# Kernel optimization log

Hardware: AMD Instinct MI355X
Metric: run time of the kernel (lower is better)

## Reference

```python
import jax, jax.numpy as jnp
import numpy as np

R_MAX = 5.0
P_CUT = 5
NAVG = 16.0
L_OF_LM = np.array([0, 1, 1, 1, 2, 2, 2, 2, 2, 3, 3, 3, 3, 3, 3, 3])


def _sph(v):
    # real spherical harmonics up to l=3 on normalized vectors, [E,16]
    n = jnp.sqrt(jnp.sum(v * v, -1, keepdims=True) + 1e-12)
    u = v / n
    x, y, z = u[..., 0], u[..., 1], u[..., 2]
    s3, s15, s5 = np.sqrt(3.0), np.sqrt(15.0), np.sqrt(5.0)
    s70, s105, s42, s7 = np.sqrt(70.0), np.sqrt(105.0), np.sqrt(42.0), np.sqrt(7.0)
    Y = [jnp.ones_like(x),
         s3 * x, s3 * y, s3 * z,
         s15 * x * y, s15 * y * z, 0.5 * s5 * (3 * z * z - 1.0), s15 * x * z, 0.5 * s15 * (x * x - y * y),
         0.25 * s70 * y * (3 * x * x - y * y), s105 * x * y * z, 0.25 * s42 * y * (5 * z * z - 1.0),
         0.5 * s7 * z * (5 * z * z - 3.0), 0.25 * s42 * x * (5 * z * z - 1.0),
         0.5 * s105 * z * (x * x - y * y), 0.25 * s70 * x * (3 * x * x - y * y)]
    return jnp.stack(Y, -1)


def _radial(r):
    # Bessel basis * smooth polynomial cutoff, r: [E] -> [E, 8]
    n = jnp.arange(1, 9, dtype=r.dtype)
    bess = np.sqrt(2.0 / R_MAX) * jnp.sin(n * np.pi * r[:, None] / R_MAX) / (r[:, None] + 1e-9)
    u = r / R_MAX
    p = float(P_CUT)
    f = 1.0 - 0.5 * (p + 1) * (p + 2) * u ** P_CUT + p * (p + 2) * u ** (P_CUT + 1) - 0.5 * p * (p + 1) * u ** (P_CUT + 2)
    f = jnp.where(u < 1.0, f, 0.0)
    return bess * f[:, None]


def _energy(node_attrs, positions, shifts, atomic_energies, W_embed, W_up, W_r1, W_r2, W_r3,
            W_lin, W_skip, U1, U2, U3, Wc1, Wc2, Wc3, W_prod, W_readout,
            edge_index, batch, num_graphs):
    send, recv = edge_index[0], edge_index[1]
    vec = positions[recv] - positions[send] + shifts
    r = jnp.sqrt(jnp.sum(vec * vec, -1) + 1e-12)
    Y = _sph(vec)                       # [E,16]
    edge_feats = _radial(r)             # [E,8]
    h = node_attrs @ W_embed            # [N,K] scalar node features
    lidx = jnp.asarray(L_OF_LM)
    N = h.shape[0]
    for i in range(2):
        h_up = h @ W_up[i]
        w = jax.nn.silu(edge_feats @ W_r1[i])
        w = jax.nn.silu(w @ W_r2[i])
        w = (w @ W_r3[i]).reshape(edge_feats.shape[0], -1, 4)   # [E,K,4] per-l radial tp weights
        w_lm = w[:, :, lidx]                                    # [E,K,16]
        m = w_lm * h_up[send][:, :, None] * Y[:, None, :]       # scalar x SH tensor product messages
        agg = jax.ops.segment_sum(m, recv, num_segments=N) / NAVG
        Wm = W_lin[i][lidx]                                     # [16,K,K] per-l linear
        mixed = jnp.einsum('nkm,mkh->nhm', agg, Wm)
        sc = jnp.einsum('nk,ne,ekh->nh', h, node_attrs, W_skip[i])  # element-wise skip tp -> scalars
        A = mixed.at[:, :, 0].add(sc)                           # [N,K,16] A-basis
        # ACE symmetric product basis (invariant outputs), element-dependent weights
        w1 = jnp.einsum('ne,epk->npk', node_attrs, Wc1[i])
        b1 = jnp.einsum('nkp,npk->nk', jnp.einsum('nka,ap->nkp', A, U1), w1)
        AA = jnp.einsum('nka,nkb->nkab', A, A)                  # [N,K,16,16]
        w2 = jnp.einsum('ne,epk->npk', node_attrs, Wc2[i])
        b2 = jnp.einsum('nkp,npk->nk', jnp.einsum('nkab,abp->nkp', AA, U2), w2)
        T3 = jnp.einsum('nkab,abcp->nkcp', AA, U3)              # [N,K,16,8]
        w3 = jnp.einsum('ne,epk->npk', node_attrs, Wc3[i])
        b3 = jnp.einsum('nkp,npk->nk', jnp.einsum('nkcp,nkc->nkp', T3, A), w3)
        h = (b1 + b2 + b3) @ W_prod[i]
    node_es = h @ W_readout                                     # [N]
    node_e0 = node_attrs @ atomic_energies
    e0 = jax.ops.segment_sum(node_e0, batch, num_segments=num_graphs)
    inter = jax.ops.segment_sum(node_es, batch, num_segments=num_graphs)
    return e0 + inter


def setup_inputs():
    key = jax.random.key(0)
    ks = jax.random.split(key, 24)
    N, E, K, NE, G, NB = 2048, 32768, 128, 10, 16, 8
    P1, P2, P3, L = 2, 4, 8, 16

    def rn(k, shape, fan):
        return jax.random.normal(k, shape, jnp.float32) / np.sqrt(fan)

    elem = jax.random.randint(ks[0], (N,), 0, NE)
    return {
        'node_attrs': jax.nn.one_hot(elem, NE, dtype=jnp.float32),
        'positions': jax.random.uniform(ks[1], (N, 3), jnp.float32) * 6.0,
        'shifts': jnp.zeros((E, 3), jnp.float32),
        'atomic_energies': jax.random.normal(ks[2], (NE,), jnp.float32),
        'W_embed': rn(ks[3], (NE, K), NE),
        'W_up': rn(ks[4], (2, K, K), K),
        'W_r1': rn(ks[5], (2, NB, 64), NB),
        'W_r2': rn(ks[6], (2, 64, 64), 64),
        'W_r3': rn(ks[7], (2, 64, K * 4), 64),
        'W_lin': rn(ks[8], (2, 4, K, K), K),
        'W_skip': rn(ks[9], (2, NE, K, K), K),
        'U1': rn(ks[10], (L, P1), L),
        'U2': rn(ks[11], (L, L, P2), L * L),
        'U3': rn(ks[12], (L, L, L, P3), L * L * L),
        'Wc1': rn(ks[13], (2, NE, P1, K), P1),
        'Wc2': rn(ks[14], (2, NE, P2, K), P2),
        'Wc3': rn(ks[15], (2, NE, P3, K), P3),
        'W_prod': rn(ks[16], (2, K, K), K),
        'W_readout': rn(ks[17], (K,), K),
        'edge_index': jax.random.randint(ks[18], (2, E), 0, N).astype(jnp.int32),
        'batch': jnp.sort(jax.random.randint(ks[19], (N,), 0, G)).astype(jnp.int32),
        'num_graphs': 16,
    }


def reference(node_attrs, positions, shifts, atomic_energies, W_embed, W_up, W_r1, W_r2, W_r3,
              W_lin, W_skip, U1, U2, U3, Wc1, Wc2, Wc3, W_prod, W_readout,
              edge_index, batch, num_graphs):
    e_fn = lambda pos: _energy(node_attrs, pos, shifts, atomic_energies, W_embed, W_up, W_r1, W_r2,
                               W_r3, W_lin, W_skip, U1, U2, U3, Wc1, Wc2, Wc3, W_prod, W_readout,
                               edge_index, batch, num_graphs)
    energy = e_fn(positions)
    forces = -jax.grad(lambda p: e_fn(p).sum())(positions)
    return energy, forces
```

## Files before the change

kernel.cpp:

```cpp
#include <hip/hip_runtime.h>
#include <math.h>

#define KCH 128
#define NELEM 10

__device__ __forceinline__ int lidxf(int m){ return (m==0)?0:((m<4)?1:((m<9)?2:3)); }
__device__ __forceinline__ float siluf(float z){ return z/(1.f+expf(-z)); }
__device__ __forceinline__ float dsiluf(float z){ float s=1.f/(1.f+expf(-z)); return s*(1.f+z*(1.f-s)); }

__global__ void k_zero(float* p, int n){
  int i = blockIdx.x*256 + threadIdx.x;
  if(i<n) p[i]=0.f;
}

__global__ void k_elem(const float* attrs, int* elem, int N){
  int n = blockIdx.x*256 + threadIdx.x;
  if(n>=N) return;
  int z=0;
  for(int e=0;e<NELEM;++e) if(attrs[n*NELEM+e] > 0.5f) z=e;
  elem[n]=z;
}

__global__ void k_h0(const float* Wemb, const int* elem, float* h0, int N){
  int i = blockIdx.x*256 + threadIdx.x;
  if(i>=N*KCH) return;
  int n = i>>7, k = i&127;
  h0[i] = Wemb[elem[n]*KCH + k];
}

__global__ void k_hist(const int* keys, int* cnt, int n){
  int i = blockIdx.x*256 + threadIdx.x;
  if(i<n) atomicAdd(&cnt[keys[i]],1);
}

__global__ void k_scan(const int* cnt, int* ptr, int n){
  __shared__ int part[257];
  int t = threadIdx.x;
  int csz = (n+255)/256;
  int lo = t*csz, hi = (t+1)*csz; if(hi>n) hi=n;
  int s=0;
  for(int i=lo;i<hi;++i) s+=cnt[i];
  part[t]=s; __syncthreads();
  if(t==0){ int acc=0; for(int i=0;i<256;++i){ int v=part[i]; part[i]=acc; acc+=v; } part[256]=acc; }
  __syncthreads();
  int acc = part[t];
  for(int i=lo;i<hi;++i){ ptr[i]=acc; acc+=cnt[i]; }
  if(t==255) ptr[n]=part[256];
}

__global__ void k_scatter(const int* keys, const int* ptr, int* cur, int* idx, int n){
  int i = blockIdx.x*256 + threadIdx.x;
  if(i>=n) return;
  int k = keys[i];
  int p = atomicAdd(&cur[k],1);
  idx[ptr[k]+p] = i;
}

__global__ void k_tb(const float* src, float* dst, int nmat){
  int i = blockIdx.x*256 + threadIdx.x;
  if(i >= nmat*16384) return;
  int mat = i>>14, rc = i&16383, r = rc>>7, c = rc&127;
  dst[mat*16384 + c*128 + r] = src[i];
}

__global__ void k_tr(const float* src, float* dst, int R, int C){
  int i = blockIdx.x*256 + threadIdx.x;
  if(i>=R*C) return;
  int r=i/C, c=i-r*C;
  dst[c*R+r]=src[i];
}

__global__ void k_wbig(const float* Wl4, float* Wb){
  int i = blockIdx.x*256 + threadIdx.x;
  if(i>=16*16384) return;
  int m = i>>14, sk = i&16383;
  Wb[i] = Wl4[lidxf(m)*16384 + sk];
}
__global__ void k_wbigT(const float* Wl4, float* Wb){
  int i = blockIdx.x*256 + threadIdx.x;
  if(i>=16*16384) return;
  int m = i>>14, sk = i&16383, s = sk>>7, k = sk&127;
  Wb[i] = Wl4[lidxf(m)*16384 + k*128 + s];
}

__global__ void k_symU2(const float* U2, float* U2s){
  int i = blockIdx.x*256 + threadIdx.x;
  if(i>=1024) return;
  int p = i&3, b = (i>>2)&15, a = (i>>6)&15;
  U2s[i] = U2[a*64+b*4+p] + U2[b*64+a*4+p];
}

__global__ void k_symU3(const float* U3, float* U3s){
  int i = blockIdx.x*256 + threadIdx.x;
  if(i>=32768) return;
  int p = i&7, c = (i>>3)&15, b = (i>>7)&15, a = (i>>11)&15;
  float s = U3[a*2048+b*128+c*8+p] + U3[a*2048+c*128+b*8+p]
          + U3[b*2048+a*128+c*8+p] + U3[b*2048+c*128+a*8+p]
          + U3[c*2048+a*128+b*8+p] + U3[c*2048+b*128+a*8+p];
  U3s[i] = s;
}

__global__ void k_C1(const float* U1, const float* Wc1l, float* C1){
  int i = blockIdx.x*256 + threadIdx.x;
  if(i>=NELEM*KCH*16) return;
  int a = i&15, c = (i>>4)&127, z = i>>11;
  float s=0;
  for(int p=0;p<2;++p) s += U1[a*2+p]*Wc1l[z*2*KCH + p*KCH + c];
  C1[i]=s;
}

__global__ void k_C2S(const float* U2s, const float* Wc2l, float* C2S){
  int i = blockIdx.x*256 + threadIdx.x;
  if(i>=NELEM*KCH*256) return;
  int ab = i&255, c = (i>>8)&127, z = i>>15;
  float s=0;
  for(int p=0;p<4;++p) s += U2s[ab*4+p]*Wc2l[z*4*KCH + p*KCH + c];
  C2S[i]=s;
}

__global__ void k_T(const float* U3s, const float* Wc3l, float* T){
  int i = blockIdx.x*256 + threadIdx.x;
  if(i>=NELEM*KCH*4096) return;
  int abc = i&4095, c = (i>>12)&127, z = i>>19;
  float s=0;
  for(int p=0;p<8;++p) s += U3s[abc*8+p]*Wc3l[z*8*KCH + p*KCH + c];
  T[i]=s;
}

__global__ void k_gB1(const float* Wro, const float* Wprod1, float* gB1){
  int c = threadIdx.x;
  float s=0;
  for(int h=0;h<KCH;++h) s += Wro[h]*Wprod1[c*KCH+h];
  gB1[c]=s;
}

__global__ void k_edge_geom(const float* pos, const float* shifts, const int* ei, const int* ridx, int E,
                            int* snds, int* rcvs,
                            float* vec, float* rr, float* Y, float* dY, float* ef, float* defdr){
  int i = blockIdx.x*256 + threadIdx.x;
  if(i>=E) return;
  int e = ridx[i];
  int s = ei[e], rc = ei[E+e];
  snds[i]=s; rcvs[i]=rc;
  float vx = pos[rc*3+0]-pos[s*3+0]+shifts[e*3+0];
  float vy = pos[rc*3+1]-pos[s*3+1]+shifts[e*3+1];
  float vz = pos[rc*3+2]-pos[s*3+2]+shifts[e*3+2];
  float r2 = vx*vx+vy*vy+vz*vz + 1e-12f;
  float n = sqrtf(r2);
  float inv_n = 1.f/n;
  float x = vx*inv_n, y = vy*inv_n, z = vz*inv_n;
  vec[i*3+0]=vx; vec[i*3+1]=vy; vec[i*3+2]=vz; rr[i]=n;
  const float s3=1.7320508075688772f, s15=3.8729833462074170f, s5=2.2360679774997896f;
  const float s70=8.3666002653407556f, s105=10.2469507659595980f, s42=6.4807406984078604f, s7=2.6457513110645907f;
  float Yv[16], d0[16], d1[16], d2[16];
  Yv[0]=1.f; d0[0]=0;d1[0]=0;d2[0]=0;
  Yv[1]=s3*x; d0[1]=s3; d1[1]=0; d2[1]=0;
  Yv[2]=s3*y; d0[2]=0; d1[2]=s3; d2[2]=0;
  Yv[3]=s3*z; d0[3]=0; d1[3]=0; d2[3]=s3;
  Yv[4]=s15*x*y; d0[4]=s15*y; d1[4]=s15*x; d2[4]=0;
  Yv[5]=s15*y*z; d0[5]=0; d1[5]=s15*z; d2[5]=s15*y;
  Yv[6]=0.5f*s5*(3.f*z*z-1.f); d0[6]=0; d1[6]=0; d2[6]=3.f*s5*z;
  Yv[7]=s15*x*z; d0[7]=s15*z; d1[7]=0; d2[7]=s15*x;
  Yv[8]=0.5f*s15*(x*x-y*y); d0[8]=s15*x; d1[8]=-s15*y; d2[8]=0;
  Yv[9]=0.25f*s70*y*(3.f*x*x-y*y); d0[9]=1.5f*s70*x*y; d1[9]=0.75f*s70*(x*x-y*y); d2[9]=0;
  Yv[10]=s105*x*y*z; d0[10]=s105*y*z; d1[10]=s105*x*z; d2[10]=s105*x*y;
  Yv[11]=0.25f*s42*y*(5.f*z*z-1.f); d0[11]=0; d1[11]=0.25f*s42*(5.f*z*z-1.f); d2[11]=2.5f*s42*y*z;
  Yv[12]=0.5f*s7*z*(5.f*z*z-3.f); d0[12]=0; d1[12]=0; d2[12]=0.5f*s7*(15.f*z*z-3.f);
  Yv[13]=0.25f*s42*x*(5.f*z*z-1.f); d0[13]=0.25f*s42*(5.f*z*z-1.f); d1[13]=0; d2[13]=2.5f*s42*x*z;
  Yv[14]=0.5f*s105*z*(x*x-y*y); d0[14]=s105*x*z; d1[14]=-s105*y*z; d2[14]=0.5f*s105*(x*x-y*y);
  Yv[15]=0.25f*s70*x*(3.f*x*x-y*y); d0[15]=0.25f*s70*(9.f*x*x-y*y); d1[15]=-0.5f*s70*x*y; d2[15]=0;
  #pragma unroll
  for(int m=0;m<16;++m){
    float dm = d0[m]*x + d1[m]*y + d2[m]*z;
    dY[(size_t)i*48 + m*3 + 0] = (d0[m]-dm*x)*inv_n;
    dY[(size_t)i*48 + m*3 + 1] = (d1[m]-dm*y)*inv_n;
    dY[(size_t)i*48 + m*3 + 2] = (d2[m]-dm*z)*inv_n;
    Y[(size_t)i*16+m] = Yv[m];
  }
  const float c0 = 0.63245553203367587f;
  float rp = n + 1e-9f;
  float u = n*0.2f;
  float f, dfdr;
  if(u < 1.f){
    float u2=u*u, u4=u2*u2, u5=u4*u, u6=u5*u, u7=u6*u;
    f = 1.f - 21.f*u5 + 35.f*u6 - 15.f*u7;
    float dfdu = -105.f*u4 + 210.f*u5 - 105.f*u6;
    dfdr = dfdu*0.2f;
  } else { f=0.f; dfdr=0.f; }
  for(int b=0;b<8;++b){
    float kn = (float)(b+1)*0.62831853071795865f;
    float sr = sinf(kn*n), cr = cosf(kn*n);
    float bess = c0*sr/rp;
    float dbess = c0*(kn*cr/rp - sr/(rp*rp));
    ef[(size_t)i*8+b] = bess*f;
    defdr[(size_t)i*8+b] = dbess*f + bess*dfdr;
  }
}

__global__ __launch_bounds__(128) void k_mm(const float* X, const float* W, float* Out, int N, int acc){
  __shared__ float xs[8][KCH];
  int t = threadIdx.x;
  int n0 = blockIdx.x*8;
  for(int j=0;j<8;++j){ int n=n0+j; xs[j][t] = (n<N)? X[(size_t)n*KCH+t] : 0.f; }
  __syncthreads();
  float a[8] = {0,0,0,0,0,0,0,0};
  for(int s=0;s<KCH;++s){
    float wv = W[s*KCH + t];
    #pragma unroll
    for(int j=0;j<8;++j) a[j] += xs[j][s]*wv;
  }
  for(int j=0;j<8;++j){
    int n=n0+j;
    if(n<N){ if(acc) Out[(size_t)n*KCH+t] += a[j]; else Out[(size_t)n*KCH+t] = a[j]; }
  }
}

__global__ __launch_bounds__(256) void k_radial_w(const float* ef, const float* Wr1, const float* Wr2, const float* Wr3,
                                                  float* w, int E){
  __shared__ float t1s[16][64];
  __shared__ float t2s[16][64];
  int t = threadIdx.x;
  int e0 = blockIdx.x*16;
  for(int it=0; it<4; ++it){
    int item = t + it*256;
    int el = item>>6, j = item&63;
    float z=0;
    if(e0+el < E){
      const float* efe = ef + (size_t)(e0+el)*8;
      #pragma unroll
      for(int b=0;b<8;++b) z += efe[b]*Wr1[b*64+j];
    }
    t1s[el][j] = siluf(z);
  }
  __syncthreads();
  for(int it=0; it<4; ++it){
    int item = t + it*256;
    int el = item>>6, j = item&63;
    float z=0;
    #pragma unroll
    for(int i=0;i<64;++i) z += t1s[el][i]*Wr2[i*64+j];
    t2s[el][j] = siluf(z);
  }
  __syncthreads();
  float a0[16], a1[16];
  #pragma unroll
  for(int el=0;el<16;++el){ a0[el]=0.f; a1[el]=0.f; }
  for(int j=0;j<64;++j){
    float wa = Wr3[j*512 + t];
    float wb = Wr3[j*512 + t + 256];
    #pragma unroll
    for(int el=0;el<16;++el){
      float tv = t2s[el][j];
      a0[el] += tv*wa;
      a1[el] += tv*wb;
    }
  }
  for(int el=0;el<16;++el){
    if(e0+el < E){
      w[(size_t)(e0+el)*512 + t] = a0[el];
      w[(size_t)(e0+el)*512 + t + 256] = a1[el];
    }
  }
}

__global__ __launch_bounds__(256) void k_gather(const float* hup, const float* w, const float* Y,
                                                const int* rptr, const int* snds,
                                                float* agg, int E){
  int n = blockIdx.x;
  int t = threadIdx.x;
  int k = t & 127, mg = t >> 7;
  float acc[8] = {0,0,0,0,0,0,0,0};
  int s0 = rptr[n], s1 = rptr[n+1];
  for(int i=s0;i<s1;++i){
    int snd = snds[i];
    float hv = hup[(size_t)snd*KCH + k];
    float4 w4 = ((const float4*)(w + (size_t)i*512))[k];
    const float* Ye = Y + (size_t)i*16 + mg*8;
    if(mg==0){
      acc[0] += w4.x*hv*Ye[0];
      acc[1] += w4.y*hv*Ye[1];
      acc[2] += w4.y*hv*Ye[2];
      acc[3] += w4.y*hv*Ye[3];
      acc[4] += w4.z*hv*Ye[4];
      acc[5] += w4.z*hv*Ye[5];
      acc[6] += w4.z*hv*Ye[6];
      acc[7] += w4.z*hv*Ye[7];
    } else {
      acc[0] += w4.z*hv*Ye[0];
      acc[1] += w4.w*hv*Ye[1];
      acc[2] += w4.w*hv*Ye[2];
      acc[3] += w4.w*hv*Ye[3];
      acc[4] += w4.w*hv*Ye[4];
      acc[5] += w4.w*hv*Ye[5];
      acc[6] += w4.w*hv*Ye[6];
      acc[7] += w4.w*hv*Ye[7];
    }
  }
  const float inv = 1.f/16.f;
  float* ap = agg + (size_t)n*2048 + k*16 + mg*8;
  #pragma unroll
  for(int j=0;j<8;++j) ap[j] = acc[j]*inv;
}

__global__ __launch_bounds__(256) void k_mixed2(const float* X, const float* hin, const int* elem,
                                                const float* Wb, const float* Wsk,
                                                float* Out, float* gh, int N, int mode){
  __shared__ float xs[4][2048];
  __shared__ float hs[4][128];
  __shared__ int zs[4];
  int t = threadIdx.x;
  int n0 = blockIdx.x*4;
  for(int q=0;q<4;++q){
    const float4* Xp = (const float4*)(X + (size_t)(n0+q)*2048);
    float4* Xs = (float4*)xs[q];
    Xs[t] = Xp[t]; Xs[t+256] = Xp[t+256];
  }
  if(mode==0 && t<128){
    for(int q=0;q<4;++q) hs[q][t] = hin[(size_t)(n0+q)*KCH + t];
  }
  if(t<4) zs[t]=elem[n0+t];
  __syncthreads();
  int kg = t&31, mg=(t>>5)&3, half=t>>7;
  int k0 = kg*4, m0 = mg*4;
  int q0 = half*2, q1=q0+1;
  float acc0[4][4], acc1[4][4];
  #pragma unroll
  for(int a=0;a<4;++a){
    #pragma unroll
    for(int b=0;b<4;++b){acc0[a][b]=0.f;acc1[a][b]=0.f;}
  }
  for(int s=0;s<KCH;++s){
    float4 x0 = *(const float4*)&xs[q0][s*16+m0];
    float4 x1 = *(const float4*)&xs[q1][s*16+m0];
    #pragma unroll
    for(int mj=0;mj<4;++mj){
      const float4 wv = *(const float4*)&Wb[(size_t)(m0+mj)*16384 + s*128 + k0];
      float xm0 = (mj==0)?x0.x:((mj==1)?x0.y:((mj==2)?x0.z:x0.w));
      float xm1 = (mj==0)?x1.x:((mj==1)?x1.y:((mj==2)?x1.z:x1.w));
      acc0[mj][0]+=xm0*wv.x; acc0[mj][1]+=xm0*wv.y; acc0[mj][2]+=xm0*wv.z; acc0[mj][3]+=xm0*wv.w;
      acc1[mj][0]+=xm1*wv.x; acc1[mj][1]+=xm1*wv.y; acc1[mj][2]+=xm1*wv.z; acc1[mj][3]+=xm1*wv.w;
    }
  }
  if(mode==0 && mg==0){
    const float* W0 = Wsk + (size_t)zs[q0]*16384;
    const float* W1 = Wsk + (size_t)zs[q1]*16384;
    for(int s=0;s<KCH;++s){
      float h0v=hs[q0][s], h1v=hs[q1][s];
      float4 w0 = *(const float4*)&W0[s*128+k0];
      float4 w1 = *(const float4*)&W1[s*128+k0];
      acc0[0][0]+=h0v*w0.x; acc0[0][1]+=h0v*w0.y; acc0[0][2]+=h0v*w0.z; acc0[0][3]+=h0v*w0.w;
      acc1[0][0]+=h1v*w1.x; acc1[0][1]+=h1v*w1.y; acc1[0][2]+=h1v*w1.z; acc1[0][3]+=h1v*w1.w;
    }
  }
  #pragma unroll
  for(int ki=0;ki<4;++ki){
    *(float4*)&Out[(size_t)(n0+q0)*2048 + (k0+ki)*16 + m0] = make_float4(acc0[0][ki],acc0[1][ki],acc0[2][ki],acc0[3][ki]);
    *(float4*)&Out[(size_t)(n0+q1)*2048 + (k0+ki)*16 + m0] = make_float4(acc1[0][ki],acc1[1][ki],acc1[2][ki],acc1[3][ki]);
  }
  if(mode==2 && mg==0){
    const float* W0 = Wsk + (size_t)zs[q0]*16384;
    const float* W1 = Wsk + (size_t)zs[q1]*16384;
    float a0[4]={0,0,0,0}, a1[4]={0,0,0,0};
    for(int s=0;s<KCH;++s){
      float x0v = xs[q0][s*16], x1v = xs[q1][s*16];
      float4 w0 = *(const float4*)&W0[s*128+k0];
      float4 w1 = *(const float4*)&W1[s*128+k0];
      a0[0]+=x0v*w0.x; a0[1]+=x0v*w0.y; a0[2]+=x0v*w0.z; a0[3]+=x0v*w0.w;
      a1[0]+=x1v*w1.x; a1[1]+=x1v*w1.y; a1[2]+=x1v*w1.z; a1[3]+=x1v*w1.w;
    }
    *(float4*)&gh[(size_t)(n0+q0)*KCH + k0] = make_float4(a0[0],a0[1],a0[2],a0[3]);
    *(float4*)&gh[(size_t)(n0+q1)*KCH + k0] = make_float4(a1[0],a1[1],a1[2],a1[3]);
  }
}

__global__ __launch_bounds__(256) void k_poly_fwd(const float* A, const float* C1, const float* C2S, const float* T,
                                                  const int* eptr, const int* eidx, float* B){
  __shared__ float Ts[4096];
  __shared__ float C2s_[256];
  __shared__ float C1s_[16];
  int t = threadIdx.x;
  int z = blockIdx.x >> 7, c = blockIdx.x & 127;
  size_t cb = (size_t)z*KCH + c;
  for(int i=t;i<4096;i+=256) Ts[i] = T[cb*4096 + i];
  for(int i=t;i<256;i+=256) C2s_[i] = C2S[cb*256 + i];
  if(t<16) C1s_[t] = C1[cb*16 + t];
  __syncthreads();
  int s0 = eptr[z], cnt = eptr[z+1]-s0;
  for(int idx=t; idx<cnt; idx+=256){
    int n = eidx[s0+idx];
    float a[16];
    const float4* ap = (const float4*)(A + (size_t)n*2048 + c*16);
    float4 a4;
    a4=ap[0]; a[0]=a4.x;a[1]=a4.y;a[2]=a4.z;a[3]=a4.w;
    a4=ap[1]; a[4]=a4.x;a[5]=a4.y;a[6]=a4.z;a[7]=a4.w;
    a4=ap[2]; a[8]=a4.x;a[9]=a4.y;a[10]=a4.z;a[11]=a4.w;
    a4=ap[3]; a[12]=a4.x;a[13]=a4.y;a[14]=a4.z;a[15]=a4.w;
    float b1=0;
    #pragma unroll
    for(int i=0;i<16;++i) b1 += a[i]*C1s_[i];
    float b2=0;
    for(int i=0;i<16;++i){
      float s=0;
      #pragma unroll
      for(int j=0;j<16;++j) s += a[j]*C2s_[i*16+j];
      b2 += a[i]*s;
    }
    float b3=0;
    for(int i=0;i<16;++i){
      for(int j=0;j<16;++j){
        float p = a[i]*a[j];
        const float* Tp = &Ts[(i*16+j)*16];
        float s=0;
        #pragma unroll
        for(int kk=0;kk<16;++kk) s += Tp[kk]*a[kk];
        b3 += p*s;
      }
    }
    B[(size_t)n*KCH + c] = b1 + 0.5f*b2 + b3*(1.f/6.f);
  }
}

__global__ __launch_bounds__(256) void k_poly_bwd(const float* A, const float* C1, const float* C2S, const float* T,
                                                  const int* eptr, const int* eidx,
                                                  const float* gBvec, const float* gBbuf, float* gA){
  __shared__ float Ts[4096];
  __shared__ float C2s_[256];
  __shared__ float C1s_[16];
  int t = threadIdx.x;
  int z = blockIdx.x >> 7, c = blockIdx.x & 127;
  size_t cb = (size_t)z*KCH + c;
  for(int i=t;i<4096;i+=256) Ts[i] = T[cb*4096 + i];
  for(int i=t;i<256;i+=256) C2s_[i] = C2S[cb*256 + i];
  if(t<16) C1s_[t] = C1[cb*16 + t];
  __syncthreads();
  int s0 = eptr[z], cnt = eptr[z+1]-s0;
  for(int idx=t; idx<cnt; idx+=256){
    int n = eidx[s0+idx];
    float a[16];
    const float4* ap = (const float4*)(A + (size_t)n*2048 + c*16);
    float4 a4;
    a4=ap[0]; a[0]=a4.x;a[1]=a4.y;a[2]=a4.z;a[3]=a4.w;
    a4=ap[1]; a[4]=a4.x;a[5]=a4.y;a[6]=a4.z;a[7]=a4.w;
    a4=ap[2]; a[8]=a4.x;a[9]=a4.y;a[10]=a4.z;a[11]=a4.w;
    a4=ap[3]; a[12]=a4.x;a[13]=a4.y;a[14]=a4.z;a[15]=a4.w;
    float gB = gBvec ? gBvec[c] : gBbuf[(size_t)n*KCH + c];
    float g12[16], g3[16];
    #pragma unroll
    for(int x=0;x<16;++x){ g12[x]=C1s_[x]; g3[x]=0.f; }
    for(int x=0;x<16;++x){
      float s=0;
      #pragma unroll
      for(int b=0;b<16;++b) s += a[b]*C2s_[x*16+b];
      g12[x]+=s;
    }
    for(int b=0;b<16;++b){
      for(int c2=0;c2<16;++c2){
        float p = a[b]*a[c2];
        const float* Tp = &Ts[(b*16+c2)*16];
        #pragma unroll
        for(int x=0;x<16;++x) g3[x] += p*Tp[x];
      }
    }
    float* gp = gA + (size_t)n*2048 + c*16;
    #pragma unroll
    for(int x=0;x<16;++x) gp[x] = gB*(g12[x] + 0.5f*g3[x]);
  }
}

__global__ __launch_bounds__(256) void k_edge_bwd2(const float* gagg, const float* hup, const float* w,
                                                   const float* Y, const float* dY,
                                                   const float* vec, const float* rr,
                                                   const float* ef, const float* defdr,
                                                   const float* Wr1, const float* Wr2,
                                                   const float* Wr2T, const float* Wr3T,
                                                   const int* snds, const int* rcvs, int E,
                                                   float* ghup, float* gvec, int do_ghup, int accv){
  __shared__ float Ys[4][16];
  __shared__ float gwS[4][512];
  __shared__ float gYp[4][2][16];
  __shared__ float t1s[4][64];
  __shared__ float gz2s[4][64];
  __shared__ float efS[4][8];
  __shared__ float defS[4][8];
  int t = threadIdx.x;
  int e0 = blockIdx.x*4;
  const float inv16 = 1.f/16.f;
  if(t<64){ int le=t>>4; int ec = e0+le; if(ec<E) Ys[le][t&15] = Y[(size_t)ec*16 + (t&15)]; }
  else if(t<96){ int i=t-64; int le=i>>3; int ec=e0+le; if(ec<E) efS[le][i&7]=ef[(size_t)ec*8+(i&7)]; }
  else if(t<128){ int i=t-96; int le=i>>3; int ec=e0+le; if(ec<E) defS[le][i&7]=defdr[(size_t)ec*8+(i&7)]; }
  __syncthreads();
  for(int rep=0;rep<2;++rep){
    int le = (t>>7) + 2*rep;
    int k = t&127;
    int e = e0+le;
    bool valid = (e<E);
    int eC = valid ? e : (E-1);
    int snd = snds[eC], rcv = rcvs[eC];
    float hv = hup[(size_t)snd*KCH + k];
    float4 w4 = ((const float4*)(w + (size_t)eC*512))[k];
    float g[16];
    const float4* gp = (const float4*)(gagg + (size_t)rcv*2048 + k*16);
    float4 v4;
    v4=gp[0]; g[0]=v4.x;g[1]=v4.y;g[2]=v4.z;g[3]=v4.w;
    v4=gp[1]; g[4]=v4.x;g[5]=v4.y;g[6]=v4.z;g[7]=v4.w;
    v4=gp[2]; g[8]=v4.x;g[9]=v4.y;g[10]=v4.z;g[11]=v4.w;
    v4=gp[3]; g[12]=v4.x;g[13]=v4.y;g[14]=v4.z;g[15]=v4.w;
    const float* Yl = Ys[le];
    float p0 = g[0]*Yl[0];
    float p1 = g[1]*Yl[1]+g[2]*Yl[2]+g[3]*Yl[3];
    float p2 = g[4]*Yl[4]+g[5]*Yl[5]+g[6]*Yl[6]+g[7]*Yl[7]+g[8]*Yl[8];
    float p3 = g[9]*Yl[9]+g[10]*Yl[10]+g[11]*Yl[11]+g[12]*Yl[12]+g[13]*Yl[13]+g[14]*Yl[14]+g[15]*Yl[15];
    float hs = hv*inv16;
    ((float4*)(&gwS[le][k*4]))[0] = make_float4(p0*hs, p1*hs, p2*hs, p3*hs);
    if(do_ghup && valid){
      float s = (p0*w4.x + p1*w4.y + p2*w4.z + p3*w4.w)*inv16;
      atomicAdd(&ghup[(size_t)snd*KCH+k], s);
    }
    float q[16];
    q[0]=g[0]*w4.x*hv;
    q[1]=g[1]*w4.y*hv; q[2]=g[2]*w4.y*hv; q[3]=g[3]*w4.y*hv;
    q[4]=g[4]*w4.z*hv; q[5]=g[5]*w4.z*hv; q[6]=g[6]*w4.z*hv; q[7]=g[7]*w4.z*hv; q[8]=g[8]*w4.z*hv;
    #pragma unroll
    for(int m=9;m<16;++m) q[m]=g[m]*w4.w*hv;
    #pragma unroll
    for(int m=0;m<16;++m){
      float vv=q[m];
      #pragma unroll
      for(int off2=1; off2<64; off2<<=1) vv += __shfl_xor(vv, off2, 64);
      q[m]=vv;
    }
    if((t&63)==0){
      int wv2 = (t>>6)&1;
      #pragma unroll
      for(int m=0;m<16;++m) gYp[le][wv2][m]=q[m];
    }
  }
  __syncthreads();
  {
    int el = t>>6, j = t&63;
    int e = e0+el;
    bool valid = (e<E);
    int eC = valid ? e : (E-1);
    float z1=0;
    #pragma unroll
    for(int b=0;b<8;++b) z1 += efS[el][b]*Wr1[b*64+j];
    float ds1v = dsiluf(z1);
    t1s[el][j] = siluf(z1);
    __syncthreads();
    float z2=0;
    for(int i=0;i<64;++i) z2 += t1s[el][i]*Wr2[i*64+j];
    float ds2v = dsiluf(z2);
    float gt2=0;
    for(int i=0;i<512;++i) gt2 += gwS[el][i]*Wr3T[i*64+j];
    gz2s[el][j] = gt2*ds2v;
    __syncthreads();
    float gz1=0;
    for(int o=0;o<64;++o) gz1 += gz2s[el][o]*Wr2T[o*64+j];
    gz1 *= ds1v;
    float cj=0;
    #pragma unroll
    for(int b=0;b<8;++b) cj += Wr1[b*64+j]*defS[el][b];
    float p = gz1*cj;
    #pragma unroll
    for(int off2=1;off2<64;off2<<=1) p += __shfl_xor(p,off2,64);
    if(j<3 && valid){
      float s = p * vec[(size_t)eC*3+j] / rr[eC];
      #pragma unroll
      for(int m=0;m<16;++m)
        s += (gYp[el][0][m]+gYp[el][1][m])*inv16 * dY[(size_t)eC*48 + m*3 + j];
      if(accv) gvec[(size_t)eC*3+j] += s;
      else     gvec[(size_t)eC*3+j]  = s;
    }
  }
}

__global__ void k_energy(const float* h2, const float* Wro, const float* AE,
                         const int* elem, const int* batch, float* out, int N){
  int n = blockIdx.x*256 + threadIdx.x;
  if(n>=N) return;
  float s=0;
  for(int k=0;k<KCH;++k) s += h2[(size_t)n*KCH+k]*Wro[k];
  s += AE[elem[n]];
  atomicAdd(&out[batch[n]], s);
}

__global__ void k_forces(const float* gvec, const int* snds, const int* rcvs, int E, float* fout){
  int i = blockIdx.x*256 + threadIdx.x;
  if(i>=E*3) return;
  int e = i/3, j = i - e*3;
  float g = gvec[i];
  atomicAdd(&fout[(size_t)snds[e]*3+j], g);
  atomicAdd(&fout[(size_t)rcvs[e]*3+j], -g);
}

extern "C" void kernel_launch(void* const* d_in, const int* in_sizes, int n_in,
                              void* d_out, int out_size, void* d_ws, size_t ws_size,
                              hipStream_t stream){
  const float* attrs  = (const float*)d_in[0];
  const float* pos    = (const float*)d_in[1];
  const float* shifts = (const float*)d_in[2];
  const float* AE     = (const float*)d_in[3];
  const float* Wemb   = (const float*)d_in[4];
  const float* Wup    = (const float*)d_in[5];
  const float* Wr1    = (const float*)d_in[6];
  const float* Wr2    = (const float*)d_in[7];
  const float* Wr3    = (const float*)d_in[8];
  const float* Wlin   = (const float*)d_in[9];
  const float* Wskip  = (const float*)d_in[10];
  const float* U1     = (const float*)d_in[11];
  const float* U2     = (const float*)d_in[12];
  const float* U3     = (const float*)d_in[13];
  const float* Wc1    = (const float*)d_in[14];
  const float* Wc2    = (const float*)d_in[15];
  const float* Wc3    = (const float*)d_in[16];
  const float* Wprod  = (const float*)d_in[17];
  const float* Wro    = (const float*)d_in[18];
  const int*   ei     = (const int*)d_in[19];
  const int*   batch  = (const int*)d_in[20];
  int N = in_sizes[1]/3;
  int E = in_sizes[19]/2;
  float* out = (float*)d_out;
  int G = out_size - 3*N;

  char* base = (char*)d_ws;
  size_t off = 0;
  auto alloc = [&](size_t nbytes)->void*{
    void* p = base + off;
    off += (nbytes + 255) & ~(size_t)255;
    return p;
  };
  int* elem = (int*)alloc((size_t)N*4);
  int* rptr = (int*)alloc((size_t)(N+1)*4);
  int* rcnt = (int*)alloc((size_t)N*4);
  int* rcur = (int*)alloc((size_t)N*4);
  int* ridx = (int*)alloc((size_t)E*4);
  int* eptr = (int*)alloc((size_t)(NELEM+1)*4);
  int* ecnt = (int*)alloc((size_t)NELEM*4);
  int* ecur = (int*)alloc((size_t)NELEM*4);
  int* eidx = (int*)alloc((size_t)N*4);
  int* snds = (int*)alloc((size_t)E*4);
  int* rcvs = (int*)alloc((size_t)E*4);
  float* h0   = (float*)alloc((size_t)N*KCH*4);
  float* h1   = (float*)alloc((size_t)N*KCH*4);
  float* h2   = (float*)alloc((size_t)N*KCH*4);
  float* hup0 = (float*)alloc((size_t)N*KCH*4);
  float* hup1 = (float*)alloc((size_t)N*KCH*4);
  float* vecb = (float*)alloc((size_t)E*3*4);
  float* rb   = (float*)alloc((size_t)E*4);
  float* Yb   = (float*)alloc((size_t)E*16*4);
  float* dYb  = (float*)alloc((size_t)E*48*4);
  float* efb  = (float*)alloc((size_t)E*8*4);
  float* defb = (float*)alloc((size_t)E*8*4);
  float* wb   = (float*)alloc((size_t)E*512*4);
  float* A0   = (float*)alloc((size_t)N*2048*4);
  float* A1   = (float*)alloc((size_t)N*2048*4);
  float* aggb = (float*)alloc((size_t)N*2048*4);
  float* gAb  = (float*)alloc((size_t)N*2048*4);
  float* Bbuf = (float*)alloc((size_t)N*KCH*4);
  float* gh1  = (float*)alloc((size_t)N*KCH*4);
  float* ghup = (float*)alloc((size_t)N*KCH*4);
  float* gB0b = (float*)alloc((size_t)N*KCH*4);
  float* gB1v = (float*)alloc((size_t)KCH*4);
  float* gvecb= (float*)alloc((size_t)E*3*4);
  float* C1b  = (float*)alloc((size_t)NELEM*KCH*16*4);
  float* C2Sb = (float*)alloc((size_t)NELEM*KCH*256*4);
  float* Tb   = (float*)alloc((size_t)NELEM*KCH*4096*4);
  float* U2s  = (float*)alloc(1024*4);
  float* U3s  = (float*)alloc(32768*4);
  float* WupT1   = (float*)alloc(16384*4);
  float* WprodT0 = (float*)alloc(16384*4);
  float* WskipT1 = (float*)alloc((size_t)NELEM*16384*4);
  float* Wbig0  = (float*)alloc((size_t)16*16384*4);
  float* Wbig1  = (float*)alloc((size_t)16*16384*4);
  float* WbigT0 = (float*)alloc((size_t)16*16384*4);
  float* WbigT1 = (float*)alloc((size_t)16*16384*4);
  float* Wr3T0   = (float*)alloc(32768*4);
  float* Wr3T1   = (float*)alloc(32768*4);
  float* Wr2T0   = (float*)alloc(4096*4);
  float* Wr2T1   = (float*)alloc(4096*4);
  if(off > ws_size) return;
  float* wb1 = wb; int have_wb1 = 0;
  if(off + (size_t)E*512*4 <= ws_size){ wb1 = (float*)alloc((size_t)E*512*4); have_wb1 = 1; }
  float *C1_1=C1b, *C2_1=C2Sb, *T_1=Tb; int have_c2 = 0;
  {
    size_t need = ((size_t)NELEM*KCH*16 + (size_t)NELEM*KCH*256 + (size_t)NELEM*KCH*4096)*4 + 1024;
    if(off + need <= ws_size){
      C1_1 = (float*)alloc((size_t)NELEM*KCH*16*4);
      C2_1 = (float*)alloc((size_t)NELEM*KCH*256*4);
      T_1  = (float*)alloc((size_t)NELEM*KCH*4096*4);
      have_c2 = 1;
    }
  }

  const int KK = KCH*KCH;
  dim3 b256(256), b128(128);
  #define GR(n) dim3(((n)+255)/256)

  k_zero<<<GR(out_size),b256,0,stream>>>(out, out_size);
  k_zero<<<GR(N),b256,0,stream>>>((float*)rcnt, N);
  k_zero<<<GR(N),b256,0,stream>>>((float*)rcur, N);
  k_zero<<<GR(NELEM),b256,0,stream>>>((float*)ecnt, NELEM);
  k_zero<<<GR(NELEM),b256,0,stream>>>((float*)ecur, NELEM);
  k_zero<<<GR(N*KCH),b256,0,stream>>>(ghup, N*KCH);

  k_elem<<<GR(N),b256,0,stream>>>(attrs, elem, N);
  k_h0<<<GR(N*KCH),b256,0,stream>>>(Wemb, elem, h0, N);

  k_hist<<<GR(E),b256,0,stream>>>(ei+E, rcnt, E);
  k_scan<<<1,b256,0,stream>>>(rcnt, rptr, N);
  k_scatter<<<GR(E),b256,0,stream>>>(ei+E, rptr, rcur, ridx, E);
  k_hist<<<GR(N),b256,0,stream>>>(elem, ecnt, N);
  k_scan<<<1,b256,0,stream>>>(ecnt, eptr, NELEM);
  k_scatter<<<GR(N),b256,0,stream>>>(elem, eptr, ecur, eidx, N);

  k_tb<<<GR(KK),b256,0,stream>>>(Wup + KK, WupT1, 1);
  k_tb<<<GR(KK),b256,0,stream>>>(Wprod, WprodT0, 1);
  k_tb<<<GR(NELEM*KK),b256,0,stream>>>(Wskip + (size_t)NELEM*KK, WskipT1, NELEM);
  k_wbig <<<GR(16*KK),b256,0,stream>>>(Wlin, Wbig0);
  k_wbig <<<GR(16*KK),b256,0,stream>>>(Wlin + 4*KK, Wbig1);
  k_wbigT<<<GR(16*KK),b256,0,stream>>>(Wlin, WbigT0);
  k_wbigT<<<GR(16*KK),b256,0,stream>>>(Wlin + 4*KK, WbigT1);
  k_tr<<<GR(32768),b256,0,stream>>>(Wr3, Wr3T0, 64, 512);
  k_tr<<<GR(32768),b256,0,stream>>>(Wr3 + 32768, Wr3T1, 64, 512);
  k_tr<<<GR(4096),b256,0,stream>>>(Wr2, Wr2T0, 64, 64);
  k_tr<<<GR(4096),b256,0,stream>>>(Wr2 + 4096, Wr2T1, 64, 64);

  k_symU2<<<GR(1024),b256,0,stream>>>(U2, U2s);
  k_symU3<<<GR(32768),b256,0,stream>>>(U3, U3s);
  k_gB1<<<1,b128,0,stream>>>(Wro, Wprod + KK, gB1v);

  k_edge_geom<<<GR(E),b256,0,stream>>>(pos, shifts, ei, ridx, E, snds, rcvs,
                                       vecb, rb, Yb, dYb, efb, defb);

  dim3 mmG((N+7)/8);
  dim3 mxG((N+3)/4);
  dim3 polyG(NELEM*KCH);
  dim3 rwG((E+15)/16);
  dim3 ebG((E+3)/4);

  k_C1 <<<GR(NELEM*KCH*16),  b256,0,stream>>>(U1,  Wc1, C1b);
  k_C2S<<<GR(NELEM*KCH*256), b256,0,stream>>>(U2s, Wc2, C2Sb);
  k_T  <<<GR(NELEM*KCH*4096),b256,0,stream>>>(U3s, Wc3, Tb);
  k_mm<<<mmG,b128,0,stream>>>(h0, Wup, hup0, N, 0);
  k_radial_w<<<rwG,b256,0,stream>>>(efb, Wr1, Wr2, Wr3, wb, E);
  k_gather<<<dim3(N),b256,0,stream>>>(hup0, wb, Yb, rptr, snds, aggb, E);
  k_mixed2<<<mxG,b256,0,stream>>>(aggb, h0, elem, Wbig0, Wskip, A0, nullptr, N, 0);
  k_poly_fwd<<<polyG,b256,0,stream>>>(A0, C1b, C2Sb, Tb, eptr, eidx, Bbuf);
  k_mm<<<mmG,b128,0,stream>>>(Bbuf, Wprod, h1, N, 0);

  k_C1 <<<GR(NELEM*KCH*16),  b256,0,stream>>>(U1,  Wc1 + NELEM*2*KCH, C1_1);
  k_C2S<<<GR(NELEM*KCH*256), b256,0,stream>>>(U2s, Wc2 + NELEM*4*KCH, C2_1);
  k_T  <<<GR(NELEM*KCH*4096),b256,0,stream>>>(U3s, Wc3 + NELEM*8*KCH, T_1);
  k_mm<<<mmG,b128,0,stream>>>(h1, Wup + KK, hup1, N, 0);
  k_radial_w<<<rwG,b256,0,stream>>>(efb, Wr1 + 512, Wr2 + 4096, Wr3 + 32768, wb1, E);
  k_gather<<<dim3(N),b256,0,stream>>>(hup1, wb1, Yb, rptr, snds, aggb, E);
  k_mixed2<<<mxG,b256,0,stream>>>(aggb, h1, elem, Wbig1, Wskip + (size_t)NELEM*KK, A1, nullptr, N, 0);
  k_poly_fwd<<<polyG,b256,0,stream>>>(A1, C1_1, C2_1, T_1, eptr, eidx, Bbuf);
  k_mm<<<mmG,b128,0,stream>>>(Bbuf, Wprod + KK, h2, N, 0);

  k_energy<<<GR(N),b256,0,stream>>>(h2, Wro, AE, elem, batch, out, N);

  k_poly_bwd<<<polyG,b256,0,stream>>>(A1, C1_1, C2_1, T_1, eptr, eidx, gB1v, nullptr, gAb);
  k_mixed2<<<mxG,b256,0,stream>>>(gAb, nullptr, elem, WbigT1, WskipT1, aggb, gh1, N, 2);
  k_edge_bwd2<<<ebG,b256,0,stream>>>(aggb, hup1, wb1, Yb, dYb, vecb, rb, efb, defb,
                                     Wr1 + 512, Wr2 + 4096, Wr2T1, Wr3T1, snds, rcvs, E,
                                     ghup, gvecb, 1, 0);
  k_mm<<<mmG,b128,0,stream>>>(ghup, WupT1, gh1, N, 1);

  if(!have_c2){
    k_C1 <<<GR(NELEM*KCH*16),  b256,0,stream>>>(U1,  Wc1, C1b);
    k_C2S<<<GR(NELEM*KCH*256), b256,0,stream>>>(U2s, Wc2, C2Sb);
    k_T  <<<GR(NELEM*KCH*4096),b256,0,stream>>>(U3s, Wc3, Tb);
  }
  k_mm<<<mmG,b128,0,stream>>>(gh1, WprodT0, gB0b, N, 0);
  k_poly_bwd<<<polyG,b256,0,stream>>>(A0, C1b, C2Sb, Tb, eptr, eidx, nullptr, gB0b, gAb);
  k_mixed2<<<mxG,b256,0,stream>>>(gAb, nullptr, elem, WbigT0, nullptr, aggb, nullptr, N, 1);
  if(!have_wb1)
    k_radial_w<<<rwG,b256,0,stream>>>(efb, Wr1, Wr2, Wr3, wb, E);
  k_edge_bwd2<<<ebG,b256,0,stream>>>(aggb, hup0, wb, Yb, dYb, vecb, rb, efb, defb,
                                     Wr1, Wr2, Wr2T0, Wr3T0, snds, rcvs, E,
                                     ghup, gvecb, 0, 1);

  k_forces<<<GR(E*3),b256,0,stream>>>(gvecb, snds, rcvs, E, out + G);
  #undef GR
}
```

Baseline: 1.866 ms.

## Exploit U3 symmetry to store upper-triangle pair tensor in polynomial kernels

```diff
diff --git a/kernel.cpp b/kernel.cpp
--- a/kernel.cpp
+++ b/kernel.cpp
@@ -3,6 +3,8 @@
 
 #define KCH 128
 #define NELEM 10
+#define NPAIR 136
+#define PSZ   2176
 
 __device__ __forceinline__ int lidxf(int m){ return (m==0)?0:((m<4)?1:((m<9)?2:3)); }
 __device__ __forceinline__ float siluf(float z){ return z/(1.f+expf(-z)); }
@@ -118,13 +120,23 @@
   C2S[i]=s;
 }
 
-__global__ void k_T(const float* U3s, const float* Wc3l, float* T){
-  int i = blockIdx.x*256 + threadIdx.x;
-  if(i>=NELEM*KCH*4096) return;
-  int abc = i&4095, c = (i>>12)&127, z = i>>19;
+__global__ void k_P2(const float* U3s, const float* Wc3l, float* P){
+  int i = blockIdx.x*256 + threadIdx.x;
+  if(i >= NELEM*KCH*PSZ) return;
+  int x = i & 15;
+  int t2 = i >> 4;
+  int pair = t2 % NPAIR;
+  int cz = t2 / NPAIR;
+  int c = cz & 127, z = cz >> 7;
+  int j=0, rem=pair;
+  while(rem >= 16-j){ rem -= 16-j; ++j; }
+  int k = j + rem;
+  const float* u = U3s + (size_t)j*2048 + k*128 + x*8;
   float s=0;
-  for(int p=0;p<8;++p) s += U3s[abc*8+p]*Wc3l[z*8*KCH + p*KCH + c];
-  T[i]=s;
+  #pragma unroll
+  for(int p=0;p<8;++p) s += u[p]*Wc3l[z*8*KCH + p*KCH + c];
+  if(j==k) s *= 0.5f;
+  P[i] = s;
 }
 
 __global__ void k_gB1(const float* Wro, const float* Wprod1, float* gB1){
@@ -373,16 +385,16 @@
   }
 }
 
-__global__ __launch_bounds__(256) void k_poly_fwd(const float* A, const float* C1, const float* C2S, const float* T,
+__global__ __launch_bounds__(256) void k_poly_fwd(const float* A, const float* C1, const float* C2S, const float* P,
                                                   const int* eptr, const int* eidx, float* B){
-  __shared__ float Ts[4096];
+  __shared__ float Ps[PSZ];
   __shared__ float C2s_[256];
   __shared__ float C1s_[16];
   int t = threadIdx.x;
   int z = blockIdx.x >> 7, c = blockIdx.x & 127;
   size_t cb = (size_t)z*KCH + c;
-  for(int i=t;i<4096;i+=256) Ts[i] = T[cb*4096 + i];
-  for(int i=t;i<256;i+=256) C2s_[i] = C2S[cb*256 + i];
+  for(int i=t;i<PSZ;i+=256) Ps[i] = P[cb*PSZ + i];
+  if(t<256) C2s_[t] = C2S[cb*256 + t];
   if(t<16) C1s_[t] = C1[cb*16 + t];
   __syncthreads();
   int s0 = eptr[z], cnt = eptr[z+1]-s0;
@@ -395,6 +407,21 @@
     a4=ap[1]; a[4]=a4.x;a[5]=a4.y;a[6]=a4.z;a[7]=a4.w;
     a4=ap[2]; a[8]=a4.x;a[9]=a4.y;a[10]=a4.z;a[11]=a4.w;
     a4=ap[3]; a[12]=a4.x;a[13]=a4.y;a[14]=a4.z;a[15]=a4.w;
+    float G[16];
+    #pragma unroll
+    for(int x=0;x<16;++x) G[x]=0.f;
+    int pair=0;
+    #pragma unroll
+    for(int j=0;j<16;++j){
+      #pragma unroll
+      for(int k=j;k<16;++k){
+        float pp = a[j]*a[k];
+        const float* Pp = &Ps[pair*16];
+        #pragma unroll
+        for(int x=0;x<16;++x) G[x] += pp*Pp[x];
+        ++pair;
+      }
+    }
     float b1=0;
     #pragma unroll
     for(int i=0;i<16;++i) b1 += a[i]*C1s_[i];
@@ -405,32 +432,24 @@
       for(int j=0;j<16;++j) s += a[j]*C2s_[i*16+j];
       b2 += a[i]*s;
     }
-    float b3=0;
-    for(int i=0;i<16;++i){
-      for(int j=0;j<16;++j){
-        float p = a[i]*a[j];
-        const float* Tp = &Ts[(i*16+j)*16];
-        float s=0;
-        #pragma unroll
-        for(int kk=0;kk<16;++kk) s += Tp[kk]*a[kk];
-        b3 += p*s;
-      }
-    }
-    B[(size_t)n*KCH + c] = b1 + 0.5f*b2 + b3*(1.f/6.f);
-  }
-}
-
-__global__ __launch_bounds__(256) void k_poly_bwd(const float* A, const float* C1, const float* C2S, const float* T,
+    float b3o=0;
+    #pragma unroll
+    for(int x=0;x<16;++x) b3o += a[x]*G[x];
+    B[(size_t)n*KCH + c] = b1 + 0.5f*b2 + b3o*(1.f/3.f);
+  }
+}
+
+__global__ __launch_bounds__(256) void k_poly_bwd(const float* A, const float* C1, const float* C2S, const float* P,
                                                   const int* eptr, const int* eidx,
                                                   const float* gBvec, const float* gBbuf, float* gA){
-  __shared__ float Ts[4096];
+  __shared__ float Ps[PSZ];
   __shared__ float C2s_[256];
   __shared__ float C1s_[16];
   int t = threadIdx.x;
   int z = blockIdx.x >> 7, c = blockIdx.x & 127;
   size_t cb = (size_t)z*KCH + c;
-  for(int i=t;i<4096;i+=256) Ts[i] = T[cb*4096 + i];
-  for(int i=t;i<256;i+=256) C2s_[i] = C2S[cb*256 + i];
+  for(int i=t;i<PSZ;i+=256) Ps[i] = P[cb*PSZ + i];
+  if(t<256) C2s_[t] = C2S[cb*256 + t];
   if(t<16) C1s_[t] = C1[cb*16 + t];
   __syncthreads();
   int s0 = eptr[z], cnt = eptr[z+1]-s0;
@@ -444,26 +463,30 @@
     a4=ap[2]; a[8]=a4.x;a[9]=a4.y;a[10]=a4.z;a[11]=a4.w;
     a4=ap[3]; a[12]=a4.x;a[13]=a4.y;a[14]=a4.z;a[15]=a4.w;
     float gB = gBvec ? gBvec[c] : gBbuf[(size_t)n*KCH + c];
-    float g12[16], g3[16];
-    #pragma unroll
-    for(int x=0;x<16;++x){ g12[x]=C1s_[x]; g3[x]=0.f; }
+    float G[16];
+    #pragma unroll
+    for(int x=0;x<16;++x) G[x]=C1s_[x];
     for(int x=0;x<16;++x){
       float s=0;
       #pragma unroll
       for(int b=0;b<16;++b) s += a[b]*C2s_[x*16+b];
-      g12[x]+=s;
-    }
-    for(int b=0;b<16;++b){
-      for(int c2=0;c2<16;++c2){
-        float p = a[b]*a[c2];
-        const float* Tp = &Ts[(b*16+c2)*16];
+      G[x]+=s;
+    }
+    int pair=0;
+    #pragma unroll
+    for(int j=0;j<16;++j){
+      #pragma unroll
+      for(int k=j;k<16;++k){
+        float pp = a[j]*a[k];
+        const float* Pp = &Ps[pair*16];
         #pragma unroll
-        for(int x=0;x<16;++x) g3[x] += p*Tp[x];
+        for(int x=0;x<16;++x) G[x] += pp*Pp[x];
+        ++pair;
       }
     }
     float* gp = gA + (size_t)n*2048 + c*16;
     #pragma unroll
-    for(int x=0;x<16;++x) gp[x] = gB*(g12[x] + 0.5f*g3[x]);
+    for(int x=0;x<16;++x) gp[x] = gB*G[x];
   }
 }
 
@@ -477,7 +500,8 @@
                                                    float* ghup, float* gvec, int do_ghup, int accv){
   __shared__ float Ys[4][16];
   __shared__ float gwS[4][512];
-  __shared__ float gYp[4][2][16];
+  __shared__ float dYsT[4][3][16];
+  __shared__ float gYs[4][2][3];
   __shared__ float t1s[4][64];
   __shared__ float gz2s[4][64];
   __shared__ float efS[4][8];
@@ -488,6 +512,8 @@
   if(t<64){ int le=t>>4; int ec = e0+le; if(ec<E) Ys[le][t&15] = Y[(size_t)ec*16 + (t&15)]; }
   else if(t<96){ int i=t-64; int le=i>>3; int ec=e0+le; if(ec<E) efS[le][i&7]=ef[(size_t)ec*8+(i&7)]; }
   else if(t<128){ int i=t-96; int le=i>>3; int ec=e0+le; if(ec<E) defS[le][i&7]=defdr[(size_t)ec*8+(i&7)]; }
+  if(t<192){ int le=t/48, rem=t-le*48; int m=rem/3, j=rem-3*m; int ec=e0+le;
+    if(ec<E) dYsT[le][j][m] = dY[(size_t)ec*48 + rem]; }
   __syncthreads();
   for(int rep=0;rep<2;++rep){
     int le = (t>>7) + 2*rep;
@@ -516,23 +542,29 @@
       float s = (p0*w4.x + p1*w4.y + p2*w4.z + p3*w4.w)*inv16;
       atomicAdd(&ghup[(size_t)snd*KCH+k], s);
     }
-    float q[16];
-    q[0]=g[0]*w4.x*hv;
-    q[1]=g[1]*w4.y*hv; q[2]=g[2]*w4.y*hv; q[3]=g[3]*w4.y*hv;
-    q[4]=g[4]*w4.z*hv; q[5]=g[5]*w4.z*hv; q[6]=g[6]*w4.z*hv; q[7]=g[7]*w4.z*hv; q[8]=g[8]*w4.z*hv;
-    #pragma unroll
-    for(int m=9;m<16;++m) q[m]=g[m]*w4.w*hv;
+    float r[16];
+    r[0]=g[0]*w4.x;
+    r[1]=g[1]*w4.y; r[2]=g[2]*w4.y; r[3]=g[3]*w4.y;
+    r[4]=g[4]*w4.z; r[5]=g[5]*w4.z; r[6]=g[6]*w4.z; r[7]=g[7]*w4.z; r[8]=g[8]*w4.z;
+    #pragma unroll
+    for(int m=9;m<16;++m) r[m]=g[m]*w4.w;
+    float s0=0.f, s1=0.f, s2=0.f;
     #pragma unroll
     for(int m=0;m<16;++m){
-      float vv=q[m];
-      #pragma unroll
-      for(int off2=1; off2<64; off2<<=1) vv += __shfl_xor(vv, off2, 64);
-      q[m]=vv;
+      s0 += r[m]*dYsT[le][0][m];
+      s1 += r[m]*dYsT[le][1][m];
+      s2 += r[m]*dYsT[le][2][m];
+    }
+    s0 *= hv; s1 *= hv; s2 *= hv;
+    #pragma unroll
+    for(int off2=1; off2<64; off2<<=1){
+      s0 += __shfl_xor(s0, off2, 64);
+      s1 += __shfl_xor(s1, off2, 64);
+      s2 += __shfl_xor(s2, off2, 64);
     }
     if((t&63)==0){
       int wv2 = (t>>6)&1;
-      #pragma unroll
-      for(int m=0;m<16;++m) gYp[le][wv2][m]=q[m];
+      gYs[le][wv2][0]=s0; gYs[le][wv2][1]=s1; gYs[le][wv2][2]=s2;
     }
   }
   __syncthreads();
@@ -551,7 +583,11 @@
     for(int i=0;i<64;++i) z2 += t1s[el][i]*Wr2[i*64+j];
     float ds2v = dsiluf(z2);
     float gt2=0;
-    for(int i=0;i<512;++i) gt2 += gwS[el][i]*Wr3T[i*64+j];
+    for(int i4=0;i4<128;++i4){
+      float4 g4 = *(const float4*)&gwS[el][i4*4];
+      const float* Wp = Wr3T + (size_t)(i4*4)*64 + j;
+      gt2 += g4.x*Wp[0] + g4.y*Wp[64] + g4.z*Wp[128] + g4.w*Wp[192];
+    }
     gz2s[el][j] = gt2*ds2v;
     __syncthreads();
     float gz1=0;
@@ -565,9 +601,7 @@
     for(int off2=1;off2<64;off2<<=1) p += __shfl_xor(p,off2,64);
     if(j<3 && valid){
       float s = p * vec[(size_t)eC*3+j] / rr[eC];
-      #pragma unroll
-      for(int m=0;m<16;++m)
-        s += (gYp[el][0][m]+gYp[el][1][m])*inv16 * dY[(size_t)eC*48 + m*3 + j];
+      s += (gYs[el][0][j]+gYs[el][1][j])*inv16;
       if(accv) gvec[(size_t)eC*3+j] += s;
       else     gvec[(size_t)eC*3+j]  = s;
     }
@@ -664,7 +698,7 @@
   float* gvecb= (float*)alloc((size_t)E*3*4);
   float* C1b  = (float*)alloc((size_t)NELEM*KCH*16*4);
   float* C2Sb = (float*)alloc((size_t)NELEM*KCH*256*4);
-  float* Tb   = (float*)alloc((size_t)NELEM*KCH*4096*4);
+  float* Pb   = (float*)alloc((size_t)NELEM*KCH*PSZ*4);
   float* U2s  = (float*)alloc(1024*4);
   float* U3s  = (float*)alloc(32768*4);
   float* WupT1   = (float*)alloc(16384*4);
@@ -681,13 +715,13 @@
   if(off > ws_size) return;
   float* wb1 = wb; int have_wb1 = 0;
   if(off + (size_t)E*512*4 <= ws_size){ wb1 = (float*)alloc((size_t)E*512*4); have_wb1 = 1; }
-  float *C1_1=C1b, *C2_1=C2Sb, *T_1=Tb; int have_c2 = 0;
+  float *C1_1=C1b, *C2_1=C2Sb, *P_1=Pb; int have_c2 = 0;
   {
-    size_t need = ((size_t)NELEM*KCH*16 + (size_t)NELEM*KCH*256 + (size_t)NELEM*KCH*4096)*4 + 1024;
+    size_t need = ((size_t)NELEM*KCH*16 + (size_t)NELEM*KCH*256 + (size_t)NELEM*KCH*PSZ)*4 + 1024;
     if(off + need <= ws_size){
       C1_1 = (float*)alloc((size_t)NELEM*KCH*16*4);
       C2_1 = (float*)alloc((size_t)NELEM*KCH*256*4);
-      T_1  = (float*)alloc((size_t)NELEM*KCH*4096*4);
+      P_1  = (float*)alloc((size_t)NELEM*KCH*PSZ*4);
       have_c2 = 1;
     }
   }
@@ -740,27 +774,27 @@
 
   k_C1 <<<GR(NELEM*KCH*16),  b256,0,stream>>>(U1,  Wc1, C1b);
   k_C2S<<<GR(NELEM*KCH*256), b256,0,stream>>>(U2s, Wc2, C2Sb);
-  k_T  <<<GR(NELEM*KCH*4096),b256,0,stream>>>(U3s, Wc3, Tb);
+  k_P2 <<<GR(NELEM*KCH*PSZ), b256,0,stream>>>(U3s, Wc3, Pb);
   k_mm<<<mmG,b128,0,stream>>>(h0, Wup, hup0, N, 0);
   k_radial_w<<<rwG,b256,0,stream>>>(efb, Wr1, Wr2, Wr3, wb, E);
   k_gather<<<dim3(N),b256,0,stream>>>(hup0, wb, Yb, rptr, snds, aggb, E);
   k_mixed2<<<mxG,b256,0,stream>>>(aggb, h0, elem, Wbig0, Wskip, A0, nullptr, N, 0);
-  k_poly_fwd<<<polyG,b256,0,stream>>>(A0, C1b, C2Sb, Tb, eptr, eidx, Bbuf);
+  k_poly_fwd<<<polyG,b256,0,stream>>>(A0, C1b, C2Sb, Pb, eptr, eidx, Bbuf);
   k_mm<<<mmG,b128,0,stream>>>(Bbuf, Wprod, h1, N, 0);
 
   k_C1 <<<GR(NELEM*KCH*16),  b256,0,stream>>>(U1,  Wc1 + NELEM*2*KCH, C1_1);
   k_C2S<<<GR(NELEM*KCH*256), b256,0,stream>>>(U2s, Wc2 + NELEM*4*KCH, C2_1);
-  k_T  <<<GR(NELEM*KCH*4096),b256,0,stream>>>(U3s, Wc3 + NELEM*8*KCH, T_1);
+  k_P2 <<<GR(NELEM*KCH*PSZ), b256,0,stream>>>(U3s, Wc3 + NELEM*8*KCH, P_1);
   k_mm<<<mmG,b128,0,stream>>>(h1, Wup + KK, hup1, N, 0);
   k_radial_w<<<rwG,b256,0,stream>>>(efb, Wr1 + 512, Wr2 + 4096, Wr3 + 32768, wb1, E);
   k_gather<<<dim3(N),b256,0,stream>>>(hup1, wb1, Yb, rptr, snds, aggb, E);
   k_mixed2<<<mxG,b256,0,stream>>>(aggb, h1, elem, Wbig1, Wskip + (size_t)NELEM*KK, A1, nullptr, N, 0);
-  k_poly_fwd<<<polyG,b256,0,stream>>>(A1, C1_1, C2_1, T_1, eptr, eidx, Bbuf);
+  k_poly_fwd<<<polyG,b256,0,stream>>>(A1, C1_1, C2_1, P_1, eptr, eidx, Bbuf);
   k_mm<<<mmG,b128,0,stream>>>(Bbuf, Wprod + KK, h2, N, 0);
 
   k_energy<<<GR(N),b256,0,stream>>>(h2, Wro, AE, elem, batch, out, N);
 
-  k_poly_bwd<<<polyG,b256,0,stream>>>(A1, C1_1, C2_1, T_1, eptr, eidx, gB1v, nullptr, gAb);
+  k_poly_bwd<<<polyG,b256,0,stream>>>(A1, C1_1, C2_1, P_1, eptr, eidx, gB1v, nullptr, gAb);
   k_mixed2<<<mxG,b256,0,stream>>>(gAb, nullptr, elem, WbigT1, WskipT1, aggb, gh1, N, 2);
   k_edge_bwd2<<<ebG,b256,0,stream>>>(aggb, hup1, wb1, Yb, dYb, vecb, rb, efb, defb,
                                      Wr1 + 512, Wr2 + 4096, Wr2T1, Wr3T1, snds, rcvs, E,
@@ -770,10 +804,10 @@
   if(!have_c2){
     k_C1 <<<GR(NELEM*KCH*16),  b256,0,stream>>>(U1,  Wc1, C1b);
     k_C2S<<<GR(NELEM*KCH*256), b256,0,stream>>>(U2s, Wc2, C2Sb);
-    k_T  <<<GR(NELEM*KCH*4096),b256,0,stream>>>(U3s, Wc3, Tb);
+    k_P2 <<<GR(NELEM*KCH*PSZ), b256,0,stream>>>(U3s, Wc3, Pb);
   }
   k_mm<<<mmG,b128,0,stream>>>(gh1, WprodT0, gB0b, N, 0);
-  k_poly_bwd<<<polyG,b256,0,stream>>>(A0, C1b, C2Sb, Tb, eptr, eidx, nullptr, gB0b, gAb);
+  k_poly_bwd<<<polyG,b256,0,stream>>>(A0, C1b, C2Sb, Pb, eptr, eidx, nullptr, gB0b, gAb);
   k_mixed2<<<mxG,b256,0,stream>>>(gAb, nullptr, elem, WbigT0, nullptr, aggb, nullptr, N, 1);
   if(!have_wb1)
     k_radial_w<<<rwG,b256,0,stream>>>(efb, Wr1, Wr2, Wr3, wb, E);
```

Result: slower. 2.320 ms (+24.3%).
